# Performance work log

Hardware: AMD Instinct MI355X
Metric: run time of the kernel (lower is better)

The kernel has to match this reference:

```python
import jax
jax.config.update("jax_enable_x64", True)
import jax.numpy as jnp
import numpy as np

SCALE = 1 << 16  # 65536 fixed-point scale
HALF = SCALE // 2

DIM = 4096
HIDDEN = 11008  # multiple_of * ceil(int(2*16384/3)/256)
TOKENS = 1024


def setup_inputs() -> dict:
    key = jax.random.key(0)
    kx, k1, k2, k3 = jax.random.split(key, 4)
    # Integer-valued fixed-point activations (torch code treats x as int32).
    x = jax.random.randint(kx, (TOKENS, DIM), 0, 256, dtype=jnp.int32)
    # Learned float weights (quantized to int32 fixed-point inside forward).
    w1 = jax.random.normal(k1, (HIDDEN, DIM), dtype=jnp.float32) * 0.02
    w2 = jax.random.normal(k2, (DIM, HIDDEN), dtype=jnp.float32) * 0.02
    w3 = jax.random.normal(k3, (HIDDEN, DIM), dtype=jnp.float32) * 0.02
    return {"x": x, "w1": w1, "w2": w2, "w3": w3}


def reference(x, w1, w2, w3):
    # Quantize weights to int32 fixed point (round half-to-even, like torch.round).
    w1i = jnp.round(w1.astype(jnp.float64) * SCALE).astype(jnp.int32)
    w2i = jnp.round(w2.astype(jnp.float64) * SCALE).astype(jnp.int32)
    w3i = jnp.round(w3.astype(jnp.float64) * SCALE).astype(jnp.int32)

    xf = x.astype(jnp.float64)  # [T, D]
    # Emulated integer GEMMs via fp64 matmul, truncated to int64 (exact here).
    t1 = jnp.matmul(xf, w1i.T.astype(jnp.float64)).astype(jnp.int64)  # [T, H]
    t3 = jnp.matmul(xf, w3i.T.astype(jnp.float64)).astype(jnp.int64)  # [T, H]

    # Requantize up-projection: rounding floor-div by SCALE (int floor division).
    q3 = ((t3 + HALF) // SCALE).astype(jnp.int32)

    # Gate path: requantize, dequantize to fp16, SiLU, re-quantize to int32.
    g = (t1 + HALF) // SCALE
    g = (g.astype(jnp.float64) / SCALE).astype(jnp.float16)
    g = jax.nn.silu(g)  # fp16 SiLU, matching F.silu on half
    g = jnp.round(g.astype(jnp.float64) * SCALE).astype(jnp.int32)

    # Fixed-point elementwise product with rounding requantization.
    t13 = ((g.astype(jnp.int64) * q3.astype(jnp.int64) + HALF) // SCALE).astype(jnp.int32)

    # Down projection GEMM + final requantization.
    t123 = jnp.matmul(t13.astype(jnp.float64), w2i.T.astype(jnp.float64)).astype(jnp.int64)
    out = ((t123 + HALF) // SCALE).astype(jnp.int32)  # [T, D]
    return out
```

## Files before the change

kernel.cpp:

```cpp
#include <hip/hip_runtime.h>
#include <hip/hip_fp16.h>
#include <math.h>

#define TOK  1024
#define DIMK 4096
#define HID  11008

typedef long long ll;
typedef int v4i  __attribute__((ext_vector_type(4)));
typedef int v16i __attribute__((ext_vector_type(16)));

#define T13_OFF 0ull
#define LUT_OFF 11272192ull
#define CS1_OFF (LUT_OFF + 32768ull)
#define CS3_OFF (CS1_OFF + 44032ull)
#define XQ_OFF  (CS3_OFF + 44032ull)
#define WQ_OFF  (XQ_OFF + 4194304ull)
#define PLANE   45088768ull
#define WS_NEED (WQ_OFF + 6ull * PLANE)

__device__ __forceinline__ int gate_requant(int g) {
  const float vf = __half2float(__float2half((float)g * (1.0f / 65536.0f)));
  const float e32 = (float)exp(-(double)vf);
  const float e16 = __half2float(__float2half(e32));
  const float d16 = __half2float(__float2half(1.0f + e16));
  const float s16 = __half2float(__float2half(1.0f / d16));
  const float p16 = __half2float(__float2half(vf * s16));
  return __float2int_rn(p16 * 65536.0f);
}

__device__ __forceinline__ v16i vzero16() {
  v16i z;
  #pragma unroll
  for (int i = 0; i < 16; ++i) z[i] = 0;
  return z;
}

__device__ __forceinline__ void gll(const void* g, void* l) {
  __builtin_amdgcn_global_load_lds((const __attribute__((address_space(1))) unsigned int*)g,
                                   (__attribute__((address_space(3))) unsigned int*)l,
                                   16, 0, 0);
}


__global__ void lut_kernel(int* __restrict__ lut) {
  const int i = blockIdx.x * blockDim.x + threadIdx.x;
  lut[i] = gate_requant(i - 4096);
}

__global__ __launch_bounds__(256)
void xq_kernel(const int* __restrict__ x, char* __restrict__ xq) {
  const size_t base = ((size_t)blockIdx.x * 256 + threadIdx.x) * 16;
  int w[4];
  #pragma unroll
  for (int i = 0; i < 4; ++i) {
    const int4 v = *reinterpret_cast<const int4*>(&x[base + i * 4]);
    w[i] = ((v.x & 255) | ((v.y & 255) << 8) | ((v.z & 255) << 16) | ((v.w & 255) << 24)) ^ 0x80808080;
  }
  *reinterpret_cast<int4*>(&xq[base]) = make_int4(w[0], w[1], w[2], w[3]);
}

__global__ __launch_bounds__(256)
void prequant_all(const float* __restrict__ w1, const float* __restrict__ w3,
                  const float* __restrict__ w2, char* __restrict__ wq,
                  int* __restrict__ cs1, int* __restrict__ cs3)
{
  const int bid = blockIdx.x;
  const int m = bid / 11008;
  const int rb = bid - m * 11008;
  const float* src = (m == 0) ? w1 : ((m == 1) ? w3 : w2);
  int* lo = (int*)(wq + (size_t)(2 * m) * PLANE);
  int* hi = (int*)(wq + (size_t)(2 * m + 1) * PLANE);
  const size_t f4base = (size_t)rb * 1024;

  int sum = 0;
  #pragma unroll
  for (int j = 0; j < 4; ++j) {
    const size_t f4 = f4base + threadIdx.x + j * 256;
    const float4 f = *reinterpret_cast<const float4*>(&src[f4 * 4]);
    const int q0 = __float2int_rn(f.x * 65536.0f);
    const int q1 = __float2int_rn(f.y * 65536.0f);
    const int q2 = __float2int_rn(f.z * 65536.0f);
    const int q3 = __float2int_rn(f.w * 65536.0f);
    sum += q0 + q1 + q2 + q3;
    lo[f4] = (q0 & 127) | ((q1 & 127) << 8) | ((q2 & 127) << 16) | ((q3 & 127) << 24);
    hi[f4] = ((q0 >> 7) & 255) | (((q1 >> 7) & 255) << 8) |
             (((q2 >> 7) & 255) << 16) | (((q3 >> 7) & 255) << 24);
  }
  if (m < 2) {
    #pragma unroll
    for (int off = 32; off > 0; off >>= 1) sum += __shfl_xor(sum, off, 64);
    if ((threadIdx.x & 63) == 0) atomicAdd(((m == 0) ? cs1 : cs3) + rb, sum);
  }
}

#define UP_BUF 32768

__global__ __launch_bounds__(512, 1)
void up_gemm(const char* __restrict__ xq, const char* __restrict__ wq,
             const int* __restrict__ csum1, const int* __restrict__ csum3,
             const int* __restrict__ lut, char* __restrict__ t13)
{
  __shared__ char smem[3 * UP_BUF];
  const int tid = threadIdx.x;
  const int w = tid >> 6, l = tid & 63;
  const int rf = w & 3, cf = w >> 2;
  const int l16 = l * 16;

  const int flat = blockIdx.x;
  const int g = (flat & 7) * 86 + (flat >> 3);
  const int col0 = (g >> 2) * 64;
  const int row0 = (g & 3) * 256;

  const char* gA = xq + (size_t)(row0 + w * 32 + (l & 31)) * DIMK + (l >> 5) * 16;
  const char* gB = wq + (size_t)(w >> 1) * PLANE
                 + (size_t)(col0 + (w & 1) * 32 + (l & 31)) * DIMK + (l >> 5) * 16;
  const unsigned dA0 = (2 * w + 0) * 1024, dA1 = (2 * w + 1) * 1024;
  const unsigned dB0 = 16384 + (2 * w + 0) * 1024, dB1 = 16384 + (2 * w + 1) * 1024;

  v16i acc[2][4];
  #pragma unroll
  for (int m = 0; m < 2; ++m)
    #pragma unroll
    for (int p = 0; p < 4; ++p) acc[m][p] = vzero16();

  gll(gA, smem + dA0);       gll(gA + 32, smem + dA1);
  gll(gB, smem + dB0);       gll(gB + 32, smem + dB1);
  gll(gA + 64, smem + UP_BUF + dA0);  gll(gA + 96, smem + UP_BUF + dA1);
  gll(gB + 64, smem + UP_BUF + dB0);  gll(gB + 96, smem + UP_BUF + dB1);
  asm volatile("s_waitcnt vmcnt(4)" ::: "memory");
  __builtin_amdgcn_s_barrier();

  const int NT = DIMK / 64;
  unsigned co = 0, so = 2 * UP_BUF;
  for (int kt = 0; kt < NT; ++kt) {
    const char* sb = smem + co;
    const bool st = (kt + 2 < NT);
    const int kb = (kt + 2) * 64;
    {
      const v4i av0 = *(const v4i*)(sb + (rf * 4 + 0) * 1024 + l16);
      const v4i av1 = *(const v4i*)(sb + (rf * 4 + 2) * 1024 + l16);
      const v4i b0  = *(const v4i*)(sb + 16384 + (0 * 4 + cf * 2) * 1024 + l16);
      const v4i b1  = *(const v4i*)(sb + 16384 + (1 * 4 + cf * 2) * 1024 + l16);
      const v4i b2  = *(const v4i*)(sb + 16384 + (2 * 4 + cf * 2) * 1024 + l16);
      const v4i b3  = *(const v4i*)(sb + 16384 + (3 * 4 + cf * 2) * 1024 + l16);
      if (st) { gll(gA + kb, smem + so + dA0); gll(gA + kb + 32, smem + so + dA1); }
      __builtin_amdgcn_s_barrier();
      asm volatile("s_waitcnt lgkmcnt(0)" ::: "memory");
      __builtin_amdgcn_sched_barrier(0);
      __builtin_amdgcn_s_setprio(1);
      acc[0][0] = __builtin_amdgcn_mfma_i32_32x32x32_i8(av0, b0, acc[0][0], 0, 0, 0);
      acc[0][1] = __builtin_amdgcn_mfma_i32_32x32x32_i8(av0, b1, acc[0][1], 0, 0, 0);
      acc[0][2] = __builtin_amdgcn_mfma_i32_32x32x32_i8(av0, b2, acc[0][2], 0, 0, 0);
      acc[0][3] = __builtin_amdgcn_mfma_i32_32x32x32_i8(av0, b3, acc[0][3], 0, 0, 0);
      acc[1][0] = __builtin_amdgcn_mfma_i32_32x32x32_i8(av1, b0, acc[1][0], 0, 0, 0);
      acc[1][1] = __builtin_amdgcn_mfma_i32_32x32x32_i8(av1, b1, acc[1][1], 0, 0, 0);
      acc[1][2] = __builtin_amdgcn_mfma_i32_32x32x32_i8(av1, b2, acc[1][2], 0, 0, 0);
      acc[1][3] = __builtin_amdgcn_mfma_i32_32x32x32_i8(av1, b3, acc[1][3], 0, 0, 0);
      __builtin_amdgcn_s_setprio(0);
      __builtin_amdgcn_s_barrier();
    }
    {
      const v4i av0 = *(const v4i*)(sb + (rf * 4 + 1) * 1024 + l16);
      const v4i av1 = *(const v4i*)(sb + (rf * 4 + 3) * 1024 + l16);
      const v4i b0  = *(const v4i*)(sb + 16384 + (0 * 4 + cf * 2 + 1) * 1024 + l16);
      const v4i b1  = *(const v4i*)(sb + 16384 + (1 * 4 + cf * 2 + 1) * 1024 + l16);
      const v4i b2  = *(const v4i*)(sb + 16384 + (2 * 4 + cf * 2 + 1) * 1024 + l16);
      const v4i b3  = *(const v4i*)(sb + 16384 + (3 * 4 + cf * 2 + 1) * 1024 + l16);
      if (st) { gll(gB + kb, smem + so + dB0); gll(gB + kb + 32, smem + so + dB1); }
      __builtin_amdgcn_s_barrier();
      asm volatile("s_waitcnt lgkmcnt(0)" ::: "memory");
      __builtin_amdgcn_sched_barrier(0);
      __builtin_amdgcn_s_setprio(1);
      acc[0][0] = __builtin_amdgcn_mfma_i32_32x32x32_i8(av0, b0, acc[0][0], 0, 0, 0);
      acc[0][1] = __builtin_amdgcn_mfma_i32_32x32x32_i8(av0, b1, acc[0][1], 0, 0, 0);
      acc[0][2] = __builtin_amdgcn_mfma_i32_32x32x32_i8(av0, b2, acc[0][2], 0, 0, 0);
      acc[0][3] = __builtin_amdgcn_mfma_i32_32x32x32_i8(av0, b3, acc[0][3], 0, 0, 0);
      acc[1][0] = __builtin_amdgcn_mfma_i32_32x32x32_i8(av1, b0, acc[1][0], 0, 0, 0);
      acc[1][1] = __builtin_amdgcn_mfma_i32_32x32x32_i8(av1, b1, acc[1][1], 0, 0, 0);
      acc[1][2] = __builtin_amdgcn_mfma_i32_32x32x32_i8(av1, b2, acc[1][2], 0, 0, 0);
      acc[1][3] = __builtin_amdgcn_mfma_i32_32x32x32_i8(av1, b3, acc[1][3], 0, 0, 0);
      __builtin_amdgcn_s_setprio(0);
      if (st) { asm volatile("s_waitcnt vmcnt(4)" ::: "memory"); }
      else    { asm volatile("s_waitcnt vmcnt(0)" ::: "memory"); }
      __builtin_amdgcn_s_barrier();
    }
    if (st) so = (so == 2 * UP_BUF) ? 0 : so + UP_BUF;
    co = (co == 2 * UP_BUF) ? 0 : co + UP_BUF;
  }

  const int col = col0 + cf * 32 + (l & 31);
  const int cs1v = csum1[col], cs3v = csum3[col];
  #pragma unroll
  for (int m = 0; m < 2; ++m) {
    #pragma unroll
    for (int r = 0; r < 16; ++r) {
      const int row = row0 + rf * 64 + m * 32 + (r & 3) + 8 * (r >> 2) + 4 * (l >> 5);
      const ll t1 = (ll)acc[m][0][r] + (((ll)acc[m][1][r] + cs1v) << 7);
      int gg = (int)((t1 + 32768) >> 16);
      gg = gg < -4096 ? -4096 : (gg > 4095 ? 4095 : gg);
      const ll t3 = (ll)acc[m][2][r] + (((ll)acc[m][3][r] + cs3v) << 7);
      const int q3 = (int)((t3 + 32768) >> 16);
      const int gate = lut[gg + 4096];
      t13[(size_t)row * HID + col] = (char)((int)(((ll)gate * q3 + 32768) >> 16));
    }
  }
}

#define DN_BUF 24576

__global__ __launch_bounds__(512, 1)
void down_gemm(const char* __restrict__ t13, const char* __restrict__ w2lo,
               const char* __restrict__ w2hi, int* __restrict__ out)
{
  __shared__ char smem[3 * DN_BUF];
  const int tid = threadIdx.x;
  const int w = tid >> 6, l = tid & 63;
  const int rf = w & 3, cf = w >> 2;
  const int l16 = l * 16;

  const int flat = blockIdx.x;
  const int g = (flat & 7) * 32 + (flat >> 3);
  const int col0 = (g >> 2) * 64;
  const int row0 = (g & 3) * 256;

  const char* gA = t13 + (size_t)(row0 + w * 32 + (l & 31)) * HID + (l >> 5) * 16;
  const char* pB = (w >> 2) ? w2hi : w2lo;
  const char* gB = pB + (size_t)(col0 + ((w >> 1) & 1) * 32 + (l & 31)) * HID
                 + (w & 1) * 32 + (l >> 5) * 16;
  const unsigned dA0 = (2 * w + 0) * 1024, dA1 = (2 * w + 1) * 1024;
  const unsigned dB = 16384 + w * 1024;

  v16i acc[2][2];
  #pragma unroll
  for (int m = 0; m < 2; ++m)
    #pragma unroll
    for (int p = 0; p < 2; ++p) acc[m][p] = vzero16();

  gll(gA, smem + dA0);  gll(gA + 32, smem + dA1);  gll(gB, smem + dB);
  gll(gA + 64, smem + DN_BUF + dA0);  gll(gA + 96, smem + DN_BUF + dA1);
  gll(gB + 64, smem + DN_BUF + dB);
  asm volatile("s_waitcnt vmcnt(3)" ::: "memory");
  __builtin_amdgcn_s_barrier();

  const int NT = HID / 64;
  unsigned co = 0, so = 2 * DN_BUF;
  for (int kt = 0; kt < NT; ++kt) {
    const char* sb = smem + co;
    const bool st = (kt + 2 < NT);
    const int kb = (kt + 2) * 64;
    {
      const v4i av0 = *(const v4i*)(sb + (rf * 4 + 0) * 1024 + l16);
      const v4i av1 = *(const v4i*)(sb + (rf * 4 + 2) * 1024 + l16);
      const v4i bL  = *(const v4i*)(sb + 16384 + (0 * 4 + cf * 2) * 1024 + l16);
      const v4i bH  = *(const v4i*)(sb + 16384 + (1 * 4 + cf * 2) * 1024 + l16);
      if (st) { gll(gA + kb, smem + so + dA0); gll(gA + kb + 32, smem + so + dA1); }
      __builtin_amdgcn_s_barrier();
      asm volatile("s_waitcnt lgkmcnt(0)" ::: "memory");
      __builtin_amdgcn_sched_barrier(0);
      __builtin_amdgcn_s_setprio(1);
      acc[0][0] = __builtin_amdgcn_mfma_i32_32x32x32_i8(av0, bL, acc[0][0], 0, 0, 0);
      acc[0][1] = __builtin_amdgcn_mfma_i32_32x32x32_i8(av0, bH, acc[0][1], 0, 0, 0);
      acc[1][0] = __builtin_amdgcn_mfma_i32_32x32x32_i8(av1, bL, acc[1][0], 0, 0, 0);
      acc[1][1] = __builtin_amdgcn_mfma_i32_32x32x32_i8(av1, bH, acc[1][1], 0, 0, 0);
      __builtin_amdgcn_s_setprio(0);
      __builtin_amdgcn_s_barrier();
    }
    {
      const v4i av0 = *(const v4i*)(sb + (rf * 4 + 1) * 1024 + l16);
      const v4i av1 = *(const v4i*)(sb + (rf * 4 + 3) * 1024 + l16);
      const v4i bL  = *(const v4i*)(sb + 16384 + (0 * 4 + cf * 2 + 1) * 1024 + l16);
      const v4i bH  = *(const v4i*)(sb + 16384 + (1 * 4 + cf * 2 + 1) * 1024 + l16);
      if (st) { gll(gB + kb, smem + so + dB); }
      __builtin_amdgcn_s_barrier();
      asm volatile("s_waitcnt lgkmcnt(0)" ::: "memory");
      __builtin_amdgcn_sched_barrier(0);
      __builtin_amdgcn_s_setprio(1);
      acc[0][0] = __builtin_amdgcn_mfma_i32_32x32x32_i8(av0, bL, acc[0][0], 0, 0, 0);
      acc[0][1] = __builtin_amdgcn_mfma_i32_32x32x32_i8(av0, bH, acc[0][1], 0, 0, 0);
      acc[1][0] = __builtin_amdgcn_mfma_i32_32x32x32_i8(av1, bL, acc[1][0], 0, 0, 0);
      acc[1][1] = __builtin_amdgcn_mfma_i32_32x32x32_i8(av1, bH, acc[1][1], 0, 0, 0);
      __builtin_amdgcn_s_setprio(0);
      if (st) { asm volatile("s_waitcnt vmcnt(3)" ::: "memory"); }
      else    { asm volatile("s_waitcnt vmcnt(0)" ::: "memory"); }
      __builtin_amdgcn_s_barrier();
    }
    if (st) so = (so == 2 * DN_BUF) ? 0 : so + DN_BUF;
    co = (co == 2 * DN_BUF) ? 0 : co + DN_BUF;
  }

  const int col = col0 + cf * 32 + (l & 31);
  #pragma unroll
  for (int m = 0; m < 2; ++m) {
    #pragma unroll
    for (int r = 0; r < 16; ++r) {
      const int row = row0 + rf * 64 + m * 32 + (r & 3) + 8 * (r >> 2) + 4 * (l >> 5);
      out[(size_t)row * DIMK + col] =
          (int)((((ll)acc[m][0][r] + ((ll)acc[m][1][r] << 7)) + 32768) >> 16);
    }
  }
}

#define BT 64
#define BN 64
#define BK 64
#define LDST 68

__device__ __forceinline__ int mad24(int a, int b, int c) {
  return ((a << 8) >> 8) * ((b << 8) >> 8) + c;
}

__global__ __launch_bounds__(256)
void ffn_up_f(const int* __restrict__ x, const float* __restrict__ w1,
              const float* __restrict__ w3, short* __restrict__ t13)
{
  __shared__ int As[BT][LDST];
  __shared__ int B1[BK][LDST];
  __shared__ int B3[BK][LDST];
  const int tx = threadIdx.x, ty = threadIdx.y;
  const int tid = ty * 16 + tx;
  const int col0 = blockIdx.x * BN;
  const int row0 = blockIdx.y * BT;
  const int lr = tid >> 4;
  const int lk = (tid & 15) << 2;
  int acc1[16] = {0};
  int acc3[16] = {0};
  for (int k0 = 0; k0 < DIMK; k0 += BK) {
    #pragma unroll
    for (int m = 0; m < 4; ++m) {
      const int r = lr + m * 16;
      *reinterpret_cast<int4*>(&As[r][lk]) =
          *reinterpret_cast<const int4*>(&x[(size_t)(row0 + r) * DIMK + k0 + lk]);
      const float4 f1 = *reinterpret_cast<const float4*>(&w1[(size_t)(col0 + r) * DIMK + k0 + lk]);
      const float4 f3 = *reinterpret_cast<const float4*>(&w3[(size_t)(col0 + r) * DIMK + k0 + lk]);
      B1[lk + 0][r] = __float2int_rn(f1.x * 65536.0f);
      B1[lk + 1][r] = __float2int_rn(f1.y * 65536.0f);
      B1[lk + 2][r] = __float2int_rn(f1.z * 65536.0f);
      B1[lk + 3][r] = __float2int_rn(f1.w * 65536.0f);
      B3[lk + 0][r] = __float2int_rn(f3.x * 65536.0f);
      B3[lk + 1][r] = __float2int_rn(f3.y * 65536.0f);
      B3[lk + 2][r] = __float2int_rn(f3.z * 65536.0f);
      B3[lk + 3][r] = __float2int_rn(f3.w * 65536.0f);
    }
    __syncthreads();
    #pragma unroll 8
    for (int kk = 0; kk < BK; ++kk) {
      const int4 b1 = *reinterpret_cast<const int4*>(&B1[kk][tx << 2]);
      const int4 b3 = *reinterpret_cast<const int4*>(&B3[kk][tx << 2]);
      #pragma unroll
      for (int i = 0; i < 4; ++i) {
        const int av = As[(ty << 2) + i][kk] & 255;
        acc1[i*4+0] = mad24(av, b1.x, acc1[i*4+0]);
        acc1[i*4+1] = mad24(av, b1.y, acc1[i*4+1]);
        acc1[i*4+2] = mad24(av, b1.z, acc1[i*4+2]);
        acc1[i*4+3] = mad24(av, b1.w, acc1[i*4+3]);
        acc3[i*4+0] = mad24(av, b3.x, acc3[i*4+0]);
        acc3[i*4+1] = mad24(av, b3.y, acc3[i*4+1]);
        acc3[i*4+2] = mad24(av, b3.z, acc3[i*4+2]);
        acc3[i*4+3] = mad24(av, b3.w, acc3[i*4+3]);
      }
    }
    __syncthreads();
  }
  #pragma unroll
  for (int i = 0; i < 4; ++i) {
    #pragma unroll
    for (int j = 0; j < 4; ++j) {
      const int g    = (acc1[i*4+j] + 32768) >> 16;
      const int q3   = (acc3[i*4+j] + 32768) >> 16;
      const int gate = gate_requant(g);
      const int tv = (int)(((ll)gate * (ll)q3 + 32768) >> 16);
      t13[(size_t)(row0 + (ty<<2) + i) * HID + col0 + (tx<<2) + j] = (short)tv;
    }
  }
}

__global__ __launch_bounds__(256)
void ffn_down_f(const short* __restrict__ t13, const float* __restrict__ w2,
                int* __restrict__ out)
{
  __shared__ int As[BT][LDST];
  __shared__ int Bs[BK][LDST];
  const int tx = threadIdx.x, ty = threadIdx.y;
  const int tid = ty * 16 + tx;
  const int col0 = blockIdx.x * BN;
  const int row0 = blockIdx.y * BT;
  const int lr = tid >> 4;
  const int lk = (tid & 15) << 2;
  const int ar = tid >> 3;
  const int ak = (tid & 7) << 3;
  int acc[16] = {0};
  for (int k0 = 0; k0 < HID; k0 += BK) {
    #pragma unroll
    for (int m = 0; m < 2; ++m) {
      const int r = ar + m * 32;
      const int4 v = *reinterpret_cast<const int4*>(&t13[(size_t)(row0 + r) * HID + k0 + ak]);
      As[r][ak+0] = (v.x << 16) >> 16;  As[r][ak+1] = v.x >> 16;
      As[r][ak+2] = (v.y << 16) >> 16;  As[r][ak+3] = v.y >> 16;
      As[r][ak+4] = (v.z << 16) >> 16;  As[r][ak+5] = v.z >> 16;
      As[r][ak+6] = (v.w << 16) >> 16;  As[r][ak+7] = v.w >> 16;
    }
    #pragma unroll
    for (int m = 0; m < 4; ++m) {
      const int r = lr + m * 16;
      const float4 f = *reinterpret_cast<const float4*>(&w2[(size_t)(col0 + r) * HID + k0 + lk]);
      Bs[lk + 0][r] = __float2int_rn(f.x * 65536.0f);
      Bs[lk + 1][r] = __float2int_rn(f.y * 65536.0f);
      Bs[lk + 2][r] = __float2int_rn(f.z * 65536.0f);
      Bs[lk + 3][r] = __float2int_rn(f.w * 65536.0f);
    }
    __syncthreads();
    #pragma unroll 8
    for (int kk = 0; kk < BK; ++kk) {
      const int4 b = *reinterpret_cast<const int4*>(&Bs[kk][tx << 2]);
      #pragma unroll
      for (int i = 0; i < 4; ++i) {
        const int av = As[(ty << 2) + i][kk];
        acc[i*4+0] = mad24(av, b.x, acc[i*4+0]);
        acc[i*4+1] = mad24(av, b.y, acc[i*4+1]);
        acc[i*4+2] = mad24(av, b.z, acc[i*4+2]);
        acc[i*4+3] = mad24(av, b.w, acc[i*4+3]);
      }
    }
    __syncthreads();
  }
  #pragma unroll
  for (int i = 0; i < 4; ++i) {
    #pragma unroll
    for (int j = 0; j < 4; ++j) {
      out[(size_t)(row0 + (ty<<2) + i) * DIMK + col0 + (tx<<2) + j] =
          (acc[i*4+j] + 32768) >> 16;
    }
  }
}

extern "C" void kernel_launch(void* const* d_in, const int* in_sizes, int n_in,
                              void* d_out, int out_size, void* d_ws, size_t ws_size,
                              hipStream_t stream) {
  (void)in_sizes; (void)n_in; (void)out_size;
  const int*   x  = (const int*)d_in[0];
  const float* w1 = (const float*)d_in[1];
  const float* w2 = (const float*)d_in[2];
  const float* w3 = (const float*)d_in[3];
  int* out = (int*)d_out;
  char* ws = (char*)d_ws;

  if (ws_size >= WS_NEED) {
    char* t13 = ws + T13_OFF;
    int*  lut = (int*)(ws + LUT_OFF);
    int*  cs1 = (int*)(ws + CS1_OFF);
    int*  cs3 = (int*)(ws + CS3_OFF);
    char* xq  = ws + XQ_OFF;
    char* wq  = ws + WQ_OFF;

    hipMemsetAsync(ws + CS1_OFF, 0, 88064, stream);
    hipLaunchKernelGGL(lut_kernel, dim3(32), dim3(256), 0, stream, lut);
    hipLaunchKernelGGL(xq_kernel, dim3(1024), dim3(256), 0, stream, x, xq);
    hipLaunchKernelGGL(prequant_all, dim3(33024), dim3(256), 0, stream,
                       w1, w3, w2, wq, cs1, cs3);
    hipLaunchKernelGGL(up_gemm, dim3(688), dim3(512), 0, stream,
                       xq, wq, cs1, cs3, lut, t13);
    hipLaunchKernelGGL(down_gemm, dim3(256), dim3(512), 0, stream,
                       t13, wq + 4 * PLANE, wq + 5 * PLANE, out);
  } else {
    if (ws_size < (size_t)TOK * HID * sizeof(short)) return;
    short* t13 = (short*)ws;
    dim3 blk(16, 16);
    hipLaunchKernelGGL(ffn_up_f,   dim3(HID / BN, TOK / BT), blk, 0, stream, x, w1, w3, t13);
    hipLaunchKernelGGL(ffn_down_f, dim3(DIMK / BN, TOK / BT), blk, 0, stream, t13, w2, out);
  }
}
```

Measured before the change: 515.5 us.

## Shrink down-GEMM tiles to 128x64 with more blocks; vectorize prequant stores

The down projection now uses 128-row by 64-column tiles instead of 256x64, so it launches 512 blocks rather than 256 and allows up to 4 blocks per CU through a smaller LDS buffer. Each wave now computes one 32x32 output with two accumulators, and load duties are split so A waves and B waves each issue two loads per stage. This aims to fill all CUs on a skinny GEMM that previously launched too few blocks, at the cost of less data reuse per tile. Separately, the weight prequant kernel gives each thread 16 contiguous floats and writes each output plane with one 16-byte store instead of four scattered 4-byte stores.

Result: slower. 571.8 us (+10.9%).

```diff
diff --git a/kernel.cpp b/kernel.cpp
--- a/kernel.cpp
+++ b/kernel.cpp
@@ -69,28 +69,32 @@
   const int m = bid / 11008;
   const int rb = bid - m * 11008;
   const float* src = (m == 0) ? w1 : ((m == 1) ? w3 : w2);
-  int* lo = (int*)(wq + (size_t)(2 * m) * PLANE);
-  int* hi = (int*)(wq + (size_t)(2 * m + 1) * PLANE);
-  const size_t f4base = (size_t)rb * 1024;
+  int4* lo = (int4*)(wq + (size_t)(2 * m) * PLANE);
+  int4* hi = (int4*)(wq + (size_t)(2 * m + 1) * PLANE);
+  const int t = threadIdx.x;
+  const size_t fbase = (size_t)rb * 4096 + (size_t)t * 16;
 
   int sum = 0;
-  #pragma unroll
-  for (int j = 0; j < 4; ++j) {
-    const size_t f4 = f4base + threadIdx.x + j * 256;
-    const float4 f = *reinterpret_cast<const float4*>(&src[f4 * 4]);
+  int lob[4], hib[4];
+  #pragma unroll
+  for (int i = 0; i < 4; ++i) {
+    const float4 f = *reinterpret_cast<const float4*>(&src[fbase + i * 4]);
     const int q0 = __float2int_rn(f.x * 65536.0f);
     const int q1 = __float2int_rn(f.y * 65536.0f);
     const int q2 = __float2int_rn(f.z * 65536.0f);
     const int q3 = __float2int_rn(f.w * 65536.0f);
     sum += q0 + q1 + q2 + q3;
-    lo[f4] = (q0 & 127) | ((q1 & 127) << 8) | ((q2 & 127) << 16) | ((q3 & 127) << 24);
-    hi[f4] = ((q0 >> 7) & 255) | (((q1 >> 7) & 255) << 8) |
+    lob[i] = (q0 & 127) | ((q1 & 127) << 8) | ((q2 & 127) << 16) | ((q3 & 127) << 24);
+    hib[i] = ((q0 >> 7) & 255) | (((q1 >> 7) & 255) << 8) |
              (((q2 >> 7) & 255) << 16) | (((q3 >> 7) & 255) << 24);
   }
+  const size_t o = (size_t)rb * 256 + t;
+  lo[o] = make_int4(lob[0], lob[1], lob[2], lob[3]);
+  hi[o] = make_int4(hib[0], hib[1], hib[2], hib[3]);
   if (m < 2) {
     #pragma unroll
     for (int off = 32; off > 0; off >>= 1) sum += __shfl_xor(sum, off, 64);
-    if ((threadIdx.x & 63) == 0) atomicAdd(((m == 0) ? cs1 : cs3) + rb, sum);
+    if ((t & 63) == 0) atomicAdd(((m == 0) ? cs1 : cs3) + rb, sum);
   }
 }
 
@@ -207,9 +211,9 @@
   }
 }
 
-#define DN_BUF 24576
-
-__global__ __launch_bounds__(512, 1)
+#define DN_BUF 16384
+
+__global__ __launch_bounds__(512, 4)
 void down_gemm(const char* __restrict__ t13, const char* __restrict__ w2lo,
                const char* __restrict__ w2hi, int* __restrict__ out)
 {
@@ -220,27 +224,27 @@
   const int l16 = l * 16;
 
   const int flat = blockIdx.x;
-  const int g = (flat & 7) * 32 + (flat >> 3);
-  const int col0 = (g >> 2) * 64;
-  const int row0 = (g & 3) * 256;
-
-  const char* gA = t13 + (size_t)(row0 + w * 32 + (l & 31)) * HID + (l >> 5) * 16;
-  const char* pB = (w >> 2) ? w2hi : w2lo;
-  const char* gB = pB + (size_t)(col0 + ((w >> 1) & 1) * 32 + (l & 31)) * HID
-                 + (w & 1) * 32 + (l >> 5) * 16;
-  const unsigned dA0 = (2 * w + 0) * 1024, dA1 = (2 * w + 1) * 1024;
-  const unsigned dB = 16384 + w * 1024;
-
-  v16i acc[2][2];
-  #pragma unroll
-  for (int m = 0; m < 2; ++m)
-    #pragma unroll
-    for (int p = 0; p < 2; ++p) acc[m][p] = vzero16();
-
-  gll(gA, smem + dA0);  gll(gA + 32, smem + dA1);  gll(gB, smem + dB);
-  gll(gA + 64, smem + DN_BUF + dA0);  gll(gA + 96, smem + DN_BUF + dA1);
-  gll(gB + 64, smem + DN_BUF + dB);
-  asm volatile("s_waitcnt vmcnt(3)" ::: "memory");
+  const int g = (flat & 7) * 64 + (flat >> 3);
+  const int col0 = (g >> 3) * 64;
+  const int row0 = (g & 7) * 128;
+
+  const char* gS;
+  unsigned dS;
+  if (w < 4) {
+    gS = t13 + (size_t)(row0 + w * 32 + (l & 31)) * HID + (l >> 5) * 16;
+    dS = (2 * w) * 1024;
+  } else {
+    const int i = w - 4;
+    const char* pB = (i >> 1) ? w2hi : w2lo;
+    gS = pB + (size_t)(col0 + (i & 1) * 32 + (l & 31)) * HID + (l >> 5) * 16;
+    dS = 8192 + (2 * i) * 1024;
+  }
+
+  v16i accL = vzero16(), accH = vzero16();
+
+  gll(gS,      smem + dS);           gll(gS + 32, smem + dS + 1024);
+  gll(gS + 64, smem + DN_BUF + dS);  gll(gS + 96, smem + DN_BUF + dS + 1024);
+  asm volatile("s_waitcnt vmcnt(2)" ::: "memory");
   __builtin_amdgcn_s_barrier();
 
   const int NT = HID / 64;
@@ -250,38 +254,32 @@
     const bool st = (kt + 2 < NT);
     const int kb = (kt + 2) * 64;
     {
-      const v4i av0 = *(const v4i*)(sb + (rf * 4 + 0) * 1024 + l16);
-      const v4i av1 = *(const v4i*)(sb + (rf * 4 + 2) * 1024 + l16);
-      const v4i bL  = *(const v4i*)(sb + 16384 + (0 * 4 + cf * 2) * 1024 + l16);
-      const v4i bH  = *(const v4i*)(sb + 16384 + (1 * 4 + cf * 2) * 1024 + l16);
-      if (st) { gll(gA + kb, smem + so + dA0); gll(gA + kb + 32, smem + so + dA1); }
+      const v4i av = *(const v4i*)(sb + (rf * 2 + 0) * 1024 + l16);
+      const v4i bL = *(const v4i*)(sb + 8192 + (0 + 2 * cf + 0) * 1024 + l16);
+      const v4i bH = *(const v4i*)(sb + 8192 + (4 + 2 * cf + 0) * 1024 + l16);
+      if (st) { gll(gS + kb, smem + so + dS); }
       __builtin_amdgcn_s_barrier();
       asm volatile("s_waitcnt lgkmcnt(0)" ::: "memory");
       __builtin_amdgcn_sched_barrier(0);
       __builtin_amdgcn_s_setprio(1);
-      acc[0][0] = __builtin_amdgcn_mfma_i32_32x32x32_i8(av0, bL, acc[0][0], 0, 0, 0);
-      acc[0][1] = __builtin_amdgcn_mfma_i32_32x32x32_i8(av0, bH, acc[0][1], 0, 0, 0);
-      acc[1][0] = __builtin_amdgcn_mfma_i32_32x32x32_i8(av1, bL, acc[1][0], 0, 0, 0);
-      acc[1][1] = __builtin_amdgcn_mfma_i32_32x32x32_i8(av1, bH, acc[1][1], 0, 0, 0);
+      accL = __builtin_amdgcn_mfma_i32_32x32x32_i8(av, bL, accL, 0, 0, 0);
+      accH = __builtin_amdgcn_mfma_i32_32x32x32_i8(av, bH, accH, 0, 0, 0);
       __builtin_amdgcn_s_setprio(0);
       __builtin_amdgcn_s_barrier();
     }
     {
-      const v4i av0 = *(const v4i*)(sb + (rf * 4 + 1) * 1024 + l16);
-      const v4i av1 = *(const v4i*)(sb + (rf * 4 + 3) * 1024 + l16);
-      const v4i bL  = *(const v4i*)(sb + 16384 + (0 * 4 + cf * 2 + 1) * 1024 + l16);
-      const v4i bH  = *(const v4i*)(sb + 16384 + (1 * 4 + cf * 2 + 1) * 1024 + l16);
-      if (st) { gll(gB + kb, smem + so + dB); }
+      const v4i av = *(const v4i*)(sb + (rf * 2 + 1) * 1024 + l16);
+      const v4i bL = *(const v4i*)(sb + 8192 + (0 + 2 * cf + 1) * 1024 + l16);
+      const v4i bH = *(const v4i*)(sb + 8192 + (4 + 2 * cf + 1) * 1024 + l16);
+      if (st) { gll(gS + kb + 32, smem + so + dS + 1024); }
       __builtin_amdgcn_s_barrier();
       asm volatile("s_waitcnt lgkmcnt(0)" ::: "memory");
       __builtin_amdgcn_sched_barrier(0);
       __builtin_amdgcn_s_setprio(1);
-      acc[0][0] = __builtin_amdgcn_mfma_i32_32x32x32_i8(av0, bL, acc[0][0], 0, 0, 0);
-      acc[0][1] = __builtin_amdgcn_mfma_i32_32x32x32_i8(av0, bH, acc[0][1], 0, 0, 0);
-      acc[1][0] = __builtin_amdgcn_mfma_i32_32x32x32_i8(av1, bL, acc[1][0], 0, 0, 0);
-      acc[1][1] = __builtin_amdgcn_mfma_i32_32x32x32_i8(av1, bH, acc[1][1], 0, 0, 0);
+      accL = __builtin_amdgcn_mfma_i32_32x32x32_i8(av, bL, accL, 0, 0, 0);
+      accH = __builtin_amdgcn_mfma_i32_32x32x32_i8(av, bH, accH, 0, 0, 0);
       __builtin_amdgcn_s_setprio(0);
-      if (st) { asm volatile("s_waitcnt vmcnt(3)" ::: "memory"); }
+      if (st) { asm volatile("s_waitcnt vmcnt(2)" ::: "memory"); }
       else    { asm volatile("s_waitcnt vmcnt(0)" ::: "memory"); }
       __builtin_amdgcn_s_barrier();
     }
@@ -291,13 +289,10 @@
 
   const int col = col0 + cf * 32 + (l & 31);
   #pragma unroll
-  for (int m = 0; m < 2; ++m) {
-    #pragma unroll
-    for (int r = 0; r < 16; ++r) {
-      const int row = row0 + rf * 64 + m * 32 + (r & 3) + 8 * (r >> 2) + 4 * (l >> 5);
-      out[(size_t)row * DIMK + col] =
-          (int)((((ll)acc[m][0][r] + ((ll)acc[m][1][r] << 7)) + 32768) >> 16);
-    }
+  for (int r = 0; r < 16; ++r) {
+    const int row = row0 + rf * 32 + (r & 3) + 8 * (r >> 2) + 4 * (l >> 5);
+    out[(size_t)row * DIMK + col] =
+        (int)((((ll)accL[r] + ((ll)accH[r] << 7)) + 32768) >> 16);
   }
 }
 
@@ -460,7 +455,7 @@
                        w1, w3, w2, wq, cs1, cs3);
     hipLaunchKernelGGL(up_gemm, dim3(688), dim3(512), 0, stream,
                        xq, wq, cs1, cs3, lut, t13);
-    hipLaunchKernelGGL(down_gemm, dim3(256), dim3(512), 0, stream,
+    hipLaunchKernelGGL(down_gemm, dim3(512), dim3(512), 0, stream,
                        t13, wq + 4 * PLANE, wq + 5 * PLANE, out);
   } else {
     if (ws_size < (size_t)TOK * HID * sizeof(short)) return;
```

## Halve up-GEMM tile rows to raise occupancy and double the block count

Applied to the files above, without the earlier changes.

The up-projection GEMM tile shrinks from 256x64 to 128x64 rows per block. Each wave now holds 4 accumulators instead of 8, LDS per stage drops from 32 KB to 24 KB, the grid doubles to 1376 blocks, and launch bounds allow 4 blocks per CU (down_gemm gets 2). The intent is more resident waves to hide latency and better load balance. In exchange, each block reuses its weight tiles across fewer rows, so global and LDS traffic per MFMA rises.

New measurement: 608.9 us. +18.1%, slower.

```diff
diff --git a/kernel.cpp b/kernel.cpp
--- a/kernel.cpp
+++ b/kernel.cpp
@@ -94,9 +94,9 @@
   }
 }
 
-#define UP_BUF 32768
-
-__global__ __launch_bounds__(512, 1)
+#define UP_BUF 24576
+
+__global__ __launch_bounds__(512, 4)
 void up_gemm(const char* __restrict__ xq, const char* __restrict__ wq,
              const int* __restrict__ csum1, const int* __restrict__ csum3,
              const int* __restrict__ lut, char* __restrict__ t13)
@@ -108,27 +108,29 @@
   const int l16 = l * 16;
 
   const int flat = blockIdx.x;
-  const int g = (flat & 7) * 86 + (flat >> 3);
-  const int col0 = (g >> 2) * 64;
-  const int row0 = (g & 3) * 256;
-
-  const char* gA = xq + (size_t)(row0 + w * 32 + (l & 31)) * DIMK + (l >> 5) * 16;
-  const char* gB = wq + (size_t)(w >> 1) * PLANE
-                 + (size_t)(col0 + (w & 1) * 32 + (l & 31)) * DIMK + (l >> 5) * 16;
-  const unsigned dA0 = (2 * w + 0) * 1024, dA1 = (2 * w + 1) * 1024;
-  const unsigned dB0 = 16384 + (2 * w + 0) * 1024, dB1 = 16384 + (2 * w + 1) * 1024;
-
-  v16i acc[2][4];
-  #pragma unroll
-  for (int m = 0; m < 2; ++m)
-    #pragma unroll
-    for (int p = 0; p < 4; ++p) acc[m][p] = vzero16();
-
-  gll(gA, smem + dA0);       gll(gA + 32, smem + dA1);
-  gll(gB, smem + dB0);       gll(gB + 32, smem + dB1);
-  gll(gA + 64, smem + UP_BUF + dA0);  gll(gA + 96, smem + UP_BUF + dA1);
-  gll(gB + 64, smem + UP_BUF + dB0);  gll(gB + 96, smem + UP_BUF + dB1);
-  asm volatile("s_waitcnt vmcnt(4)" ::: "memory");
+  const int g = (flat & 7) * 172 + (flat >> 3);
+  const int col0 = (g >> 3) * 64;
+  const int row0 = (g & 7) * 128;
+
+  const char* gA = xq + (size_t)(row0 + (w >> 1) * 32 + (l & 31)) * DIMK
+                 + (w & 1) * 32 + (l >> 5) * 16;
+  const int t0 = 2 * w, t1 = 2 * w + 1;
+  const char* gB0 = wq + (size_t)(t0 >> 2) * PLANE
+      + (size_t)(col0 + ((t0 >> 1) & 1) * 32 + (l & 31)) * DIMK + (t0 & 1) * 32 + (l >> 5) * 16;
+  const char* gB1 = wq + (size_t)(t1 >> 2) * PLANE
+      + (size_t)(col0 + ((t1 >> 1) & 1) * 32 + (l & 31)) * DIMK + (t1 & 1) * 32 + (l >> 5) * 16;
+  const unsigned dA  = w * 1024;
+  const unsigned dB0 = 8192 + t0 * 1024, dB1 = 8192 + t1 * 1024;
+
+  v16i acc[4];
+  #pragma unroll
+  for (int p = 0; p < 4; ++p) acc[p] = vzero16();
+
+  gll(gA, smem + dA);  gll(gB0, smem + dB0);  gll(gB1, smem + dB1);
+  gll(gA + 64, smem + UP_BUF + dA);
+  gll(gB0 + 64, smem + UP_BUF + dB0);
+  gll(gB1 + 64, smem + UP_BUF + dB1);
+  asm volatile("s_waitcnt vmcnt(3)" ::: "memory");
   __builtin_amdgcn_s_barrier();
 
   const int NT = DIMK / 64;
@@ -138,50 +140,40 @@
     const bool st = (kt + 2 < NT);
     const int kb = (kt + 2) * 64;
     {
-      const v4i av0 = *(const v4i*)(sb + (rf * 4 + 0) * 1024 + l16);
-      const v4i av1 = *(const v4i*)(sb + (rf * 4 + 2) * 1024 + l16);
-      const v4i b0  = *(const v4i*)(sb + 16384 + (0 * 4 + cf * 2) * 1024 + l16);
-      const v4i b1  = *(const v4i*)(sb + 16384 + (1 * 4 + cf * 2) * 1024 + l16);
-      const v4i b2  = *(const v4i*)(sb + 16384 + (2 * 4 + cf * 2) * 1024 + l16);
-      const v4i b3  = *(const v4i*)(sb + 16384 + (3 * 4 + cf * 2) * 1024 + l16);
-      if (st) { gll(gA + kb, smem + so + dA0); gll(gA + kb + 32, smem + so + dA1); }
+      const v4i av = *(const v4i*)(sb + (rf * 2 + 0) * 1024 + l16);
+      const v4i b0 = *(const v4i*)(sb + 8192 + (0 * 4 + cf * 2 + 0) * 1024 + l16);
+      const v4i b1 = *(const v4i*)(sb + 8192 + (1 * 4 + cf * 2 + 0) * 1024 + l16);
+      const v4i b2 = *(const v4i*)(sb + 8192 + (2 * 4 + cf * 2 + 0) * 1024 + l16);
+      const v4i b3 = *(const v4i*)(sb + 8192 + (3 * 4 + cf * 2 + 0) * 1024 + l16);
+      if (st) { gll(gA + kb, smem + so + dA); gll(gB0 + kb, smem + so + dB0); }
       __builtin_amdgcn_s_barrier();
       asm volatile("s_waitcnt lgkmcnt(0)" ::: "memory");
       __builtin_amdgcn_sched_barrier(0);
       __builtin_amdgcn_s_setprio(1);
-      acc[0][0] = __builtin_amdgcn_mfma_i32_32x32x32_i8(av0, b0, acc[0][0], 0, 0, 0);
-      acc[0][1] = __builtin_amdgcn_mfma_i32_32x32x32_i8(av0, b1, acc[0][1], 0, 0, 0);
-      acc[0][2] = __builtin_amdgcn_mfma_i32_32x32x32_i8(av0, b2, acc[0][2], 0, 0, 0);
-      acc[0][3] = __builtin_amdgcn_mfma_i32_32x32x32_i8(av0, b3, acc[0][3], 0, 0, 0);
-      acc[1][0] = __builtin_amdgcn_mfma_i32_32x32x32_i8(av1, b0, acc[1][0], 0, 0, 0);
-      acc[1][1] = __builtin_amdgcn_mfma_i32_32x32x32_i8(av1, b1, acc[1][1], 0, 0, 0);
-      acc[1][2] = __builtin_amdgcn_mfma_i32_32x32x32_i8(av1, b2, acc[1][2], 0, 0, 0);
-      acc[1][3] = __builtin_amdgcn_mfma_i32_32x32x32_i8(av1, b3, acc[1][3], 0, 0, 0);
+      acc[0] = __builtin_amdgcn_mfma_i32_32x32x32_i8(av, b0, acc[0], 0, 0, 0);
+      acc[1] = __builtin_amdgcn_mfma_i32_32x32x32_i8(av, b1, acc[1], 0, 0, 0);
+      acc[2] = __builtin_amdgcn_mfma_i32_32x32x32_i8(av, b2, acc[2], 0, 0, 0);
+      acc[3] = __builtin_amdgcn_mfma_i32_32x32x32_i8(av, b3, acc[3], 0, 0, 0);
       __builtin_amdgcn_s_setprio(0);
       __builtin_amdgcn_s_barrier();
     }
     {
-      const v4i av0 = *(const v4i*)(sb + (rf * 4 + 1) * 1024 + l16);
-      const v4i av1 = *(const v4i*)(sb + (rf * 4 + 3) * 1024 + l16);
-      const v4i b0  = *(const v4i*)(sb + 16384 + (0 * 4 + cf * 2 + 1) * 1024 + l16);
-      const v4i b1  = *(const v4i*)(sb + 16384 + (1 * 4 + cf * 2 + 1) * 1024 + l16);
-      const v4i b2  = *(const v4i*)(sb + 16384 + (2 * 4 + cf * 2 + 1) * 1024 + l16);
-      const v4i b3  = *(const v4i*)(sb + 16384 + (3 * 4 + cf * 2 + 1) * 1024 + l16);
-      if (st) { gll(gB + kb, smem + so + dB0); gll(gB + kb + 32, smem + so + dB1); }
+      const v4i av = *(const v4i*)(sb + (rf * 2 + 1) * 1024 + l16);
+      const v4i b0 = *(const v4i*)(sb + 8192 + (0 * 4 + cf * 2 + 1) * 1024 + l16);
+      const v4i b1 = *(const v4i*)(sb + 8192 + (1 * 4 + cf * 2 + 1) * 1024 + l16);
+      const v4i b2 = *(const v4i*)(sb + 8192 + (2 * 4 + cf * 2 + 1) * 1024 + l16);
+      const v4i b3 = *(const v4i*)(sb + 8192 + (3 * 4 + cf * 2 + 1) * 1024 + l16);
+      if (st) { gll(gB1 + kb, smem + so + dB1); }
       __builtin_amdgcn_s_barrier();
       asm volatile("s_waitcnt lgkmcnt(0)" ::: "memory");
       __builtin_amdgcn_sched_barrier(0);
       __builtin_amdgcn_s_setprio(1);
-      acc[0][0] = __builtin_amdgcn_mfma_i32_32x32x32_i8(av0, b0, acc[0][0], 0, 0, 0);
-      acc[0][1] = __builtin_amdgcn_mfma_i32_32x32x32_i8(av0, b1, acc[0][1], 0, 0, 0);
-      acc[0][2] = __builtin_amdgcn_mfma_i32_32x32x32_i8(av0, b2, acc[0][2], 0, 0, 0);
-      acc[0][3] = __builtin_amdgcn_mfma_i32_32x32x32_i8(av0, b3, acc[0][3], 0, 0, 0);
-      acc[1][0] = __builtin_amdgcn_mfma_i32_32x32x32_i8(av1, b0, acc[1][0], 0, 0, 0);
-      acc[1][1] = __builtin_amdgcn_mfma_i32_32x32x32_i8(av1, b1, acc[1][1], 0, 0, 0);
-      acc[1][2] = __builtin_amdgcn_mfma_i32_32x32x32_i8(av1, b2, acc[1][2], 0, 0, 0);
-      acc[1][3] = __builtin_amdgcn_mfma_i32_32x32x32_i8(av1, b3, acc[1][3], 0, 0, 0);
+      acc[0] = __builtin_amdgcn_mfma_i32_32x32x32_i8(av, b0, acc[0], 0, 0, 0);
+      acc[1] = __builtin_amdgcn_mfma_i32_32x32x32_i8(av, b1, acc[1], 0, 0, 0);
+      acc[2] = __builtin_amdgcn_mfma_i32_32x32x32_i8(av, b2, acc[2], 0, 0, 0);
+      acc[3] = __builtin_amdgcn_mfma_i32_32x32x32_i8(av, b3, acc[3], 0, 0, 0);
       __builtin_amdgcn_s_setprio(0);
-      if (st) { asm volatile("s_waitcnt vmcnt(4)" ::: "memory"); }
+      if (st) { asm volatile("s_waitcnt vmcnt(3)" ::: "memory"); }
       else    { asm volatile("s_waitcnt vmcnt(0)" ::: "memory"); }
       __builtin_amdgcn_s_barrier();
     }
@@ -192,24 +184,21 @@
   const int col = col0 + cf * 32 + (l & 31);
   const int cs1v = csum1[col], cs3v = csum3[col];
   #pragma unroll
-  for (int m = 0; m < 2; ++m) {
-    #pragma unroll
-    for (int r = 0; r < 16; ++r) {
-      const int row = row0 + rf * 64 + m * 32 + (r & 3) + 8 * (r >> 2) + 4 * (l >> 5);
-      const ll t1 = (ll)acc[m][0][r] + (((ll)acc[m][1][r] + cs1v) << 7);
-      int gg = (int)((t1 + 32768) >> 16);
-      gg = gg < -4096 ? -4096 : (gg > 4095 ? 4095 : gg);
-      const ll t3 = (ll)acc[m][2][r] + (((ll)acc[m][3][r] + cs3v) << 7);
-      const int q3 = (int)((t3 + 32768) >> 16);
-      const int gate = lut[gg + 4096];
-      t13[(size_t)row * HID + col] = (char)((int)(((ll)gate * q3 + 32768) >> 16));
-    }
+  for (int r = 0; r < 16; ++r) {
+    const int row = row0 + rf * 32 + (r & 3) + 8 * (r >> 2) + 4 * (l >> 5);
+    const ll t1 = (ll)acc[0][r] + (((ll)acc[1][r] + cs1v) << 7);
+    int gg = (int)((t1 + 32768) >> 16);
+    gg = gg < -4096 ? -4096 : (gg > 4095 ? 4095 : gg);
+    const ll t3 = (ll)acc[2][r] + (((ll)acc[3][r] + cs3v) << 7);
+    const int q3 = (int)((t3 + 32768) >> 16);
+    const int gate = lut[gg + 4096];
+    t13[(size_t)row * HID + col] = (char)((int)(((ll)gate * q3 + 32768) >> 16));
   }
 }
 
 #define DN_BUF 24576
 
-__global__ __launch_bounds__(512, 1)
+__global__ __launch_bounds__(512, 2)
 void down_gemm(const char* __restrict__ t13, const char* __restrict__ w2lo,
                const char* __restrict__ w2hi, int* __restrict__ out)
 {
@@ -458,7 +447,7 @@
     hipLaunchKernelGGL(xq_kernel, dim3(1024), dim3(256), 0, stream, x, xq);
     hipLaunchKernelGGL(prequant_all, dim3(33024), dim3(256), 0, stream,
                        w1, w3, w2, wq, cs1, cs3);
-    hipLaunchKernelGGL(up_gemm, dim3(688), dim3(512), 0, stream,
+    hipLaunchKernelGGL(up_gemm, dim3(1376), dim3(512), 0, stream,
                        xq, wq, cs1, cs3, lut, t13);
     hipLaunchKernelGGL(down_gemm, dim3(256), dim3(512), 0, stream,
                        t13, wq + 4 * PLANE, wq + 5 * PLANE, out);
```
